# Performance work log

Measured on AMD Instinct MI355X. Metric: run time of the kernel, lower is better.

## Reference

```python
import jax, jax.numpy as jnp
import numpy as np

N_NODES = 100000
N_EDGES = 1600000
D_IN = 128
D_HID = 128
D_OUT = 32


def setup_inputs() -> dict:
    key = jax.random.key(0)
    ks = jax.random.split(key, 10)
    x = jax.random.normal(ks[0], (N_NODES, D_IN), dtype=jnp.float32)
    edge_index = jax.random.randint(ks[1], (2, N_EDGES), 0, N_NODES, dtype=jnp.int64)
    s = 0.05
    return {
        "x": x,
        "edge_index": edge_index,
        "Wl0": jax.random.normal(ks[2], (D_IN, D_HID), jnp.float32) * s,
        "bl0": jnp.zeros((D_HID,), jnp.float32),
        "Wr0": jax.random.normal(ks[3], (D_IN, D_HID), jnp.float32) * s,
        "Wl1": jax.random.normal(ks[4], (D_HID, D_HID), jnp.float32) * s,
        "bl1": jnp.zeros((D_HID,), jnp.float32),
        "Wr1": jax.random.normal(ks[5], (D_HID, D_HID), jnp.float32) * s,
        "Wl2": jax.random.normal(ks[6], (D_HID, D_OUT), jnp.float32) * s,
        "bl2": jnp.zeros((D_OUT,), jnp.float32),
        "Wr2": jax.random.normal(ks[7], (D_HID, D_OUT), jnp.float32) * s,
    }


def _sage_conv(x, src, dst, Wl, bl, Wr):
    # PyG SAGEConv (aggr='mean', root_weight=True):
    # out[i] = lin_l(mean_{j in N(i)} x_j) + lin_r(x_i)
    n = x.shape[0]
    msgs = x[src]                                        # [E, F] gather
    agg = jax.ops.segment_sum(msgs, dst, num_segments=n) # [N, F] scatter-add
    deg = jax.ops.segment_sum(jnp.ones((src.shape[0],), x.dtype), dst, num_segments=n)
    mean = agg / jnp.maximum(deg, 1.0)[:, None]
    return mean @ Wl + bl + x @ Wr


def reference(x, edge_index, Wl0, bl0, Wr0, Wl1, bl1, Wr1, Wl2, bl2, Wr2):
    src, dst = edge_index[0], edge_index[1]
    h = jax.nn.relu(_sage_conv(x, src, dst, Wl0, bl0, Wr0))
    h = jax.nn.relu(_sage_conv(h, src, dst, Wl1, bl1, Wr1))
    h = _sage_conv(h, src, dst, Wl2, bl2, Wr2)
    return jax.nn.log_softmax(h, axis=1)
```

## Files before the change

### kernel.cpp

```cpp
#include <hip/hip_runtime.h>
#include <hip/hip_bf16.h>
#include <math.h>

#define NN 100000
#define NE 1600000

#define NCB 391
#define EB  8192
#define SCT 512

typedef __attribute__((ext_vector_type(8))) short short8;
typedef __attribute__((ext_vector_type(4))) float f32x4;

__device__ __forceinline__ unsigned short f2bf(float f) {
  union { float f; unsigned int i; } v; v.f = f;
  unsigned int i = v.i;
  unsigned int r = (i + 0x7FFFu + ((i >> 16) & 1u)) >> 16;
  return (unsigned short)r;
}
__device__ __forceinline__ float bflo(unsigned int u) {
  union { unsigned int i; float f; } v; v.i = u << 16; return v.f;
}
__device__ __forceinline__ float bfhi(unsigned int u) {
  union { unsigned int i; float f; } v; v.i = u & 0xFFFF0000u; return v.f;
}
__device__ __forceinline__ float bf1(unsigned short u) {
  union { unsigned int i; float f; } v; v.i = ((unsigned int)u) << 16; return v.f;
}

__global__ __launch_bounds__(512) void k_chist(const int* __restrict__ dst,
                                               int* __restrict__ ccnt) {
  __shared__ int h[NCB];
  for (int i = threadIdx.x; i < NCB; i += 512) h[i] = 0;
  __syncthreads();
  int stride = gridDim.x * 512;
  for (int e = blockIdx.x * 512 + threadIdx.x; e < NE; e += stride) {
    int d = dst[e];
    d = d < 0 ? 0 : (d >= NN ? NN - 1 : d);
    atomicAdd(&h[d >> 8], 1);
  }
  __syncthreads();
  for (int i = threadIdx.x; i < NCB; i += 512) {
    int v = h[i];
    if (v) atomicAdd(&ccnt[i], v);
  }
}

__global__ __launch_bounds__(512) void k_cscan(const int* __restrict__ ccnt,
                                               int* __restrict__ cboff,
                                               int* __restrict__ csroff) {
  __shared__ int sd[512];
  int t = threadIdx.x;
  int v = (t < NCB) ? ccnt[t] : 0;
  sd[t] = v;
  __syncthreads();
  for (int st = 1; st < 512; st <<= 1) {
    int x = (t >= st) ? sd[t - st] : 0;
    __syncthreads();
    sd[t] += x;
    __syncthreads();
  }
  if (t < NCB) cboff[t] = sd[t] - v;
  if (t == NCB - 1) { cboff[NCB] = sd[t]; csroff[NN] = sd[t]; }
}

__global__ __launch_bounds__(SCT) void k_cscatter(
    const int* __restrict__ src, const int* __restrict__ dst,
    const int* __restrict__ cboff, int* __restrict__ ccur,
    unsigned int* __restrict__ ebuf) {
  __shared__ int lh[NCB];
  unsigned int cbr[16], pv[16];
  int t = threadIdx.x;
  int base = blockIdx.x * EB;
  for (int i = t; i < NCB; i += SCT) lh[i] = 0;
  __syncthreads();
  #pragma unroll
  for (int i = 0; i < 16; i++) {
    int e = base + i * SCT + t;
    if (e < NE) {
      int d = dst[e];
      d = d < 0 ? 0 : (d >= NN ? NN - 1 : d);
      int s = src[e];
      s = s < 0 ? 0 : (s >= NN ? NN - 1 : s);
      int cb = d >> 8;
      int r = atomicAdd(&lh[cb], 1);
      cbr[i] = (((unsigned int)cb) << 13) | (unsigned int)r;
      pv[i]  = (((unsigned int)(d & 255)) << 17) | (unsigned int)s;
    } else {
      cbr[i] = 0xFFFFFFFFu;
    }
  }
  __syncthreads();
  for (int i = t; i < NCB; i += SCT) {
    int c = lh[i];
    int g = c ? atomicAdd(&ccur[i], c) : 0;
    lh[i] = cboff[i] + g;
  }
  __syncthreads();
  #pragma unroll
  for (int i = 0; i < 16; i++) {
    if (cbr[i] != 0xFFFFFFFFu) {
      int cb = cbr[i] >> 13;
      int r  = cbr[i] & 0x1FFF;
      ebuf[lh[cb] + r] = pv[i];
    }
  }
}

__global__ __launch_bounds__(256) void k_crefine(
    const unsigned int* __restrict__ ebuf, const int* __restrict__ cboff,
    int* __restrict__ csroff, float* __restrict__ invd,
    int* __restrict__ csrsrc) {
  __shared__ int lh[256], pos[256], cur[256];
  int b = blockIdx.x, t = threadIdx.x;
  lh[t] = 0; cur[t] = 0;
  __syncthreads();
  int beg = cboff[b], end = cboff[b + 1];
  for (int i = beg + t; i < end; i += 256) atomicAdd(&lh[ebuf[i] >> 17], 1);
  __syncthreads();
  int v = lh[t];
  pos[t] = v;
  __syncthreads();
  for (int st = 1; st < 256; st <<= 1) {
    int x = (t >= st) ? pos[t - st] : 0;
    __syncthreads();
    pos[t] += x;
    __syncthreads();
  }
  int nid = b * 256 + t;
  int mybase = cboff[b] + pos[t] - v;
  if (nid < NN) {
    csroff[nid] = mybase;
    invd[nid] = 1.0f / (float)(v < 1 ? 1 : v);
  }
  __syncthreads();
  pos[t] = mybase;
  __syncthreads();
  for (int i = beg + t; i < end; i += 256) {
    unsigned int u = ebuf[i];
    int local = u >> 17;
    int r = atomicAdd(&cur[local], 1);
    csrsrc[pos[local] + r] = (int)(u & 0x1FFFFu);
  }
}

__global__ void k_wprep(const float* __restrict__ Wl, const float* __restrict__ Wr,
                        int nch, unsigned short* __restrict__ B) {
  int idx = blockIdx.x * 256 + threadIdx.x;
  int total = 2 * nch * 128;
  if (idx < total) {
    int n = idx >> 7;
    int k = idx & 127;
    float v = (n < nch) ? Wl[k * nch + n] : Wr[k * nch + (n - nch)];
    B[idx] = f2bf(v);
  }
}

template <int NC, int AFP32>
__global__ __launch_bounds__(512) void k_mgemm(
    const void* __restrict__ Ap, const unsigned short* __restrict__ Bp,
    const float* __restrict__ bias,
    unsigned short* __restrict__ yl, unsigned short* __restrict__ yr) {
  __shared__ unsigned short sA[128 * 136];
  __shared__ unsigned short sB[NC * 136];
  int tid = threadIdx.x;
  int nb  = blockIdx.x * 128;

  if (AFP32) {
    const float* A = (const float*)Ap;
    #pragma unroll
    for (int i = 0; i < 8; i++) {
      int j = i * 512 + tid;
      int m = j >> 5;
      int k4 = (j & 31) * 4;
      int gn = nb + m;
      float4 v = make_float4(0.f, 0.f, 0.f, 0.f);
      if (gn < NN) v = *(const float4*)&A[gn * 128 + k4];
      unsigned int p0 = (unsigned int)f2bf(v.x) | ((unsigned int)f2bf(v.y) << 16);
      unsigned int p1 = (unsigned int)f2bf(v.z) | ((unsigned int)f2bf(v.w) << 16);
      *(uint2*)&sA[m * 136 + k4] = make_uint2(p0, p1);
    }
  } else {
    const unsigned short* A = (const unsigned short*)Ap;
    #pragma unroll
    for (int i = 0; i < 4; i++) {
      int j = i * 512 + tid;
      int m = j >> 4;
      int k8 = (j & 15) * 8;
      int gn = nb + m;
      uint4 v = make_uint4(0, 0, 0, 0);
      if (gn < NN) v = *(const uint4*)&A[gn * 128 + k8];
      *(uint4*)&sA[m * 136 + k8] = v;
    }
  }
  {
    int nchunks = NC * 16;
    for (int j = tid; j < nchunks; j += 512) {
      int n = j >> 4;
      int k8 = (j & 15) * 8;
      *(uint4*)&sB[n * 136 + k8] = *(const uint4*)&Bp[n * 128 + k8];
    }
  }
  __syncthreads();

  int wave = tid >> 6, lane = tid & 63;
  int l15 = lane & 15, lq = lane >> 4;
  constexpr int MT = (NC == 256) ? 4 : 2;
  constexpr int NT = (NC == 256) ? 4 : 2;
  int wm, wn;
  if (NC == 256) { wm = wave & 1; wn = wave >> 1; }
  else           { wm = wave >> 1; wn = wave & 1; }
  int mbase = wm * (MT * 16);
  int nbase = wn * (NT * 16);

  f32x4 acc[MT][NT];
  #pragma unroll
  for (int mi = 0; mi < MT; mi++)
    #pragma unroll
    for (int ni = 0; ni < NT; ni++) acc[mi][ni] = (f32x4){0.f, 0.f, 0.f, 0.f};

  #pragma unroll
  for (int kc = 0; kc < 4; kc++) {
    int k0 = kc * 32 + lq * 8;
    short8 af[MT], bfr[NT];
    #pragma unroll
    for (int mi = 0; mi < MT; mi++)
      af[mi] = *(const short8*)&sA[(mbase + mi * 16 + l15) * 136 + k0];
    #pragma unroll
    for (int ni = 0; ni < NT; ni++)
      bfr[ni] = *(const short8*)&sB[(nbase + ni * 16 + l15) * 136 + k0];
    #pragma unroll
    for (int mi = 0; mi < MT; mi++)
      #pragma unroll
      for (int ni = 0; ni < NT; ni++)
        acc[mi][ni] = __builtin_amdgcn_mfma_f32_16x16x32_bf16(
            af[mi], bfr[ni], acc[mi][ni], 0, 0, 0);
  }

  constexpr int HC = NC / 2;
  #pragma unroll
  for (int mi = 0; mi < MT; mi++) {
    #pragma unroll
    for (int ni = 0; ni < NT; ni++) {
      int n = nbase + ni * 16 + l15;
      #pragma unroll
      for (int r = 0; r < 4; r++) {
        int gn = nb + mbase + mi * 16 + lq * 4 + r;
        if (gn < NN) {
          float v = acc[mi][ni][r];
          if (n < HC) {
            yl[(size_t)gn * HC + n] = f2bf(v);
          } else {
            int n2 = n - HC;
            yr[(size_t)gn * HC + n2] = f2bf(v + bias[n2]);
          }
        }
      }
    }
  }
}

__global__ __launch_bounds__(256) void k_agg128(
    const unsigned short* __restrict__ yl, const unsigned short* __restrict__ yr,
    const int* __restrict__ off, const int* __restrict__ csr,
    const float* __restrict__ invd, unsigned short* __restrict__ out, int relu) {
  int wid  = (blockIdx.x * 256 + threadIdx.x) >> 6;
  int lane = threadIdx.x & 63;
  if (wid >= NN) return;
  int beg = off[wid], end = off[wid + 1];
  const unsigned int* ylp = (const unsigned int*)yl;
  float ax0 = 0.f, ay0 = 0.f, ax1 = 0.f, ay1 = 0.f;
  float ax2 = 0.f, ay2 = 0.f, ax3 = 0.f, ay3 = 0.f;
  int e = beg;
  for (; e + 7 < end; e += 8) {
    int s0 = csr[e],     s1 = csr[e + 1], s2 = csr[e + 2], s3 = csr[e + 3];
    int s4 = csr[e + 4], s5 = csr[e + 5], s6 = csr[e + 6], s7 = csr[e + 7];
    unsigned int u0 = ylp[s0 * 64 + lane];
    unsigned int u1 = ylp[s1 * 64 + lane];
    unsigned int u2 = ylp[s2 * 64 + lane];
    unsigned int u3 = ylp[s3 * 64 + lane];
    unsigned int u4 = ylp[s4 * 64 + lane];
    unsigned int u5 = ylp[s5 * 64 + lane];
    unsigned int u6 = ylp[s6 * 64 + lane];
    unsigned int u7 = ylp[s7 * 64 + lane];
    ax0 += bflo(u0); ay0 += bfhi(u0);
    ax1 += bflo(u1); ay1 += bfhi(u1);
    ax2 += bflo(u2); ay2 += bfhi(u2);
    ax3 += bflo(u3); ay3 += bfhi(u3);
    ax0 += bflo(u4); ay0 += bfhi(u4);
    ax1 += bflo(u5); ay1 += bfhi(u5);
    ax2 += bflo(u6); ay2 += bfhi(u6);
    ax3 += bflo(u7); ay3 += bfhi(u7);
  }
  for (; e < end; e++) {
    int s = csr[e];
    unsigned int u = ylp[s * 64 + lane];
    ax0 += bflo(u); ay0 += bfhi(u);
  }
  float sc = invd[wid];
  unsigned int rv = ((const unsigned int*)yr)[wid * 64 + lane];
  float vx = ((ax0 + ax1) + (ax2 + ax3)) * sc + bflo(rv);
  float vy = ((ay0 + ay1) + (ay2 + ay3)) * sc + bfhi(rv);
  if (relu) { vx = fmaxf(vx, 0.f); vy = fmaxf(vy, 0.f); }
  ((unsigned int*)out)[wid * 64 + lane] =
      (unsigned int)f2bf(vx) | ((unsigned int)f2bf(vy) << 16);
}

__global__ __launch_bounds__(256) void k_agg32_lsm(
    const unsigned short* __restrict__ yl, const unsigned short* __restrict__ yr,
    const int* __restrict__ off, const int* __restrict__ csr,
    const float* __restrict__ invd, float* __restrict__ out) {
  int row  = (blockIdx.x * 256 + threadIdx.x) >> 5;
  int lane = threadIdx.x & 31;
  if (row >= NN) return;
  int beg = off[row], end = off[row + 1];
  float a0 = 0.f, a1 = 0.f, a2 = 0.f, a3 = 0.f;
  int e = beg;
  for (; e + 3 < end; e += 4) {
    int s0 = csr[e], s1 = csr[e + 1], s2 = csr[e + 2], s3 = csr[e + 3];
    a0 += bf1(yl[s0 * 32 + lane]);
    a1 += bf1(yl[s1 * 32 + lane]);
    a2 += bf1(yl[s2 * 32 + lane]);
    a3 += bf1(yl[s3 * 32 + lane]);
  }
  for (; e < end; e++) a0 += bf1(yl[csr[e] * 32 + lane]);
  float v = ((a0 + a1) + (a2 + a3)) * invd[row] + bf1(yr[row * 32 + lane]);
  float m = v;
  #pragma unroll
  for (int o = 16; o; o >>= 1) m = fmaxf(m, __shfl_xor(m, o, 32));
  float ex = expf(v - m);
  float s = ex;
  #pragma unroll
  for (int o = 16; o; o >>= 1) s += __shfl_xor(s, o, 32);
  out[row * 32 + lane] = v - m - logf(s);
}


extern "C" void kernel_launch(void* const* d_in, const int* in_sizes, int n_in,
                              void* d_out, int out_size, void* d_ws, size_t ws_size,
                              hipStream_t stream) {
  (void)in_sizes; (void)n_in; (void)out_size; (void)ws_size;
  const float* x   = (const float*)d_in[0];
  const int*   ei  = (const int*)d_in[1];
  const float* Wl0 = (const float*)d_in[2];
  const float* bl0 = (const float*)d_in[3];
  const float* Wr0 = (const float*)d_in[4];
  const float* Wl1 = (const float*)d_in[5];
  const float* bl1 = (const float*)d_in[6];
  const float* Wr1 = (const float*)d_in[7];
  const float* Wl2 = (const float*)d_in[8];
  const float* bl2 = (const float*)d_in[9];
  const float* Wr2 = (const float*)d_in[10];
  const int* srcI = ei;
  const int* dstI = ei + NE;

  char* w = (char*)d_ws;
  int*   ccnt   = (int*)(w + 0);
  int*   ccur   = (int*)(w + (16 << 10));
  int*   cboff  = (int*)(w + (32 << 10));
  unsigned short* B0 = (unsigned short*)(w + (64 << 10));
  unsigned short* B1 = (unsigned short*)(w + (160 << 10));
  unsigned short* B2 = (unsigned short*)(w + (256 << 10));
  int*   csroff = (int*)(w + (512 << 10));
  float* invd   = (float*)(w + (1024 << 10));
  unsigned int* ebuf = (unsigned int*)(w + (size_t)(2) * 1024 * 1024);
  int*   csrsrc = (int*)(w + (size_t)(9) * 1024 * 1024);
  unsigned short* ylb = (unsigned short*)(w + (size_t)(16) * 1024 * 1024);
  unsigned short* yrb = (unsigned short*)(w + (size_t)(48) * 1024 * 1024);
  unsigned short* hb  = (unsigned short*)(w + (size_t)(80) * 1024 * 1024);

  hipMemsetAsync(ccnt, 0, NCB * sizeof(int), stream);
  hipMemsetAsync(ccur, 0, NCB * sizeof(int), stream);

  k_chist<<<128, 512, 0, stream>>>(dstI, ccnt);
  k_cscan<<<1, 512, 0, stream>>>(ccnt, cboff, csroff);
  k_cscatter<<<(NE + EB - 1) / EB, SCT, 0, stream>>>(srcI, dstI, cboff, ccur, ebuf);
  k_crefine<<<NCB, 256, 0, stream>>>(ebuf, cboff, csroff, invd, csrsrc);

  k_wprep<<<(2 * 128 * 128 + 255) / 256, 256, 0, stream>>>(Wl0, Wr0, 128, B0);
  k_wprep<<<(2 * 128 * 128 + 255) / 256, 256, 0, stream>>>(Wl1, Wr1, 128, B1);
  k_wprep<<<(2 * 32 * 128 + 255) / 256, 256, 0, stream>>>(Wl2, Wr2, 32, B2);

  dim3 gg((NN + 127) / 128);
  k_mgemm<256, 1><<<gg, 512, 0, stream>>>(x, B0, bl0, ylb, yrb);
  k_agg128<<<(NN * 64) / 256, 256, 0, stream>>>(ylb, yrb, csroff, csrsrc, invd, hb, 1);
  k_mgemm<256, 0><<<gg, 512, 0, stream>>>(hb, B1, bl1, ylb, yrb);
  k_agg128<<<(NN * 64) / 256, 256, 0, stream>>>(ylb, yrb, csroff, csrsrc, invd, hb, 1);
  k_mgemm<64, 0><<<gg, 512, 0, stream>>>(hb, B2, bl2, ylb, yrb);
  k_agg32_lsm<<<(NN * 32) / 256, 256, 0, stream>>>(ylb, yrb, csroff, csrsrc, invd,
                                                   (float*)d_out);
}
```

Before: 485.4 us.

## Drop memsets via per-block histograms, merge weight prep, deepen gather unroll

Each histogram block now writes its own partial counts, which the scan kernel sums. The scan kernel also zeroes the cursor array, so both memsets and the global atomics go away. The three weight-prep launches become one. The scatter kernel keeps its rank and payload in shared memory instead of registers. The aggregation kernels unroll the neighbour gather to 16 (or 8), use nontemporal loads for CSR indices and nontemporal stores for outputs, trading register/LDS pressure for more loads in flight.

Result: slower. 497.7 us (+2.5%).

```diff
diff --git a/kernel.cpp b/kernel.cpp
--- a/kernel.cpp
+++ b/kernel.cpp
@@ -8,6 +8,7 @@
 #define NCB 391
 #define EB  8192
 #define SCT 512
+#define HBK 128
 
 typedef __attribute__((ext_vector_type(8))) short short8;
 typedef __attribute__((ext_vector_type(4))) float f32x4;
@@ -29,29 +30,39 @@
 }
 
 __global__ __launch_bounds__(512) void k_chist(const int* __restrict__ dst,
-                                               int* __restrict__ ccnt) {
+                                               int* __restrict__ part) {
   __shared__ int h[NCB];
   for (int i = threadIdx.x; i < NCB; i += 512) h[i] = 0;
   __syncthreads();
-  int stride = gridDim.x * 512;
+  int stride = HBK * 512;
   for (int e = blockIdx.x * 512 + threadIdx.x; e < NE; e += stride) {
     int d = dst[e];
     d = d < 0 ? 0 : (d >= NN ? NN - 1 : d);
     atomicAdd(&h[d >> 8], 1);
   }
   __syncthreads();
-  for (int i = threadIdx.x; i < NCB; i += 512) {
-    int v = h[i];
-    if (v) atomicAdd(&ccnt[i], v);
-  }
-}
-
-__global__ __launch_bounds__(512) void k_cscan(const int* __restrict__ ccnt,
+  for (int i = threadIdx.x; i < NCB; i += 512) part[blockIdx.x * NCB + i] = h[i];
+}
+
+__global__ __launch_bounds__(512) void k_cscan(const int* __restrict__ part,
                                                int* __restrict__ cboff,
+                                               int* __restrict__ ccur,
                                                int* __restrict__ csroff) {
   __shared__ int sd[512];
   int t = threadIdx.x;
-  int v = (t < NCB) ? ccnt[t] : 0;
+  int v = 0;
+  if (t < NCB) {
+    int s0 = 0, s1 = 0, s2 = 0, s3 = 0;
+    #pragma unroll 4
+    for (int k = 0; k < HBK; k += 4) {
+      s0 += part[(k + 0) * NCB + t];
+      s1 += part[(k + 1) * NCB + t];
+      s2 += part[(k + 2) * NCB + t];
+      s3 += part[(k + 3) * NCB + t];
+    }
+    v = (s0 + s1) + (s2 + s3);
+    ccur[t] = 0;
+  }
   sd[t] = v;
   __syncthreads();
   for (int st = 1; st < 512; st <<= 1) {
@@ -69,14 +80,17 @@
     const int* __restrict__ cboff, int* __restrict__ ccur,
     unsigned int* __restrict__ ebuf) {
   __shared__ int lh[NCB];
-  unsigned int cbr[16], pv[16];
+  __shared__ unsigned int sRank[EB];
+  __shared__ unsigned int sPay[EB];
   int t = threadIdx.x;
   int base = blockIdx.x * EB;
   for (int i = t; i < NCB; i += SCT) lh[i] = 0;
   __syncthreads();
   #pragma unroll
-  for (int i = 0; i < 16; i++) {
-    int e = base + i * SCT + t;
+  for (int i = 0; i < EB / SCT; i++) {
+    int idx = i * SCT + t;
+    int e = base + idx;
+    unsigned int rk = 0xFFFFFFFFu, pv = 0;
     if (e < NE) {
       int d = dst[e];
       d = d < 0 ? 0 : (d >= NN ? NN - 1 : d);
@@ -84,11 +98,11 @@
       s = s < 0 ? 0 : (s >= NN ? NN - 1 : s);
       int cb = d >> 8;
       int r = atomicAdd(&lh[cb], 1);
-      cbr[i] = (((unsigned int)cb) << 13) | (unsigned int)r;
-      pv[i]  = (((unsigned int)(d & 255)) << 17) | (unsigned int)s;
-    } else {
-      cbr[i] = 0xFFFFFFFFu;
-    }
+      rk = (((unsigned int)cb) << 13) | (unsigned int)r;
+      pv = (((unsigned int)(d & 255)) << 17) | (unsigned int)s;
+    }
+    sRank[idx] = rk;
+    sPay[idx]  = pv;
   }
   __syncthreads();
   for (int i = t; i < NCB; i += SCT) {
@@ -98,11 +112,13 @@
   }
   __syncthreads();
   #pragma unroll
-  for (int i = 0; i < 16; i++) {
-    if (cbr[i] != 0xFFFFFFFFu) {
-      int cb = cbr[i] >> 13;
-      int r  = cbr[i] & 0x1FFF;
-      ebuf[lh[cb] + r] = pv[i];
+  for (int i = 0; i < EB / SCT; i++) {
+    int idx = i * SCT + t;
+    unsigned int rk = sRank[idx];
+    if (rk != 0xFFFFFFFFu) {
+      int cb = rk >> 13;
+      int r  = rk & 0x1FFF;
+      ebuf[lh[cb] + r] = sPay[idx];
     }
   }
 }
@@ -144,15 +160,27 @@
   }
 }
 
-__global__ void k_wprep(const float* __restrict__ Wl, const float* __restrict__ Wr,
-                        int nch, unsigned short* __restrict__ B) {
+__global__ void k_wprep(const float* __restrict__ Wl0, const float* __restrict__ Wr0,
+                        const float* __restrict__ Wl1, const float* __restrict__ Wr1,
+                        const float* __restrict__ Wl2, const float* __restrict__ Wr2,
+                        unsigned short* __restrict__ B0,
+                        unsigned short* __restrict__ B1,
+                        unsigned short* __restrict__ B2) {
   int idx = blockIdx.x * 256 + threadIdx.x;
-  int total = 2 * nch * 128;
-  if (idx < total) {
-    int n = idx >> 7;
-    int k = idx & 127;
-    float v = (n < nch) ? Wl[k * nch + n] : Wr[k * nch + (n - nch)];
-    B[idx] = f2bf(v);
+  if (idx < 32768) {
+    int n = idx >> 7, k = idx & 127;
+    float v = (n < 128) ? Wl0[k * 128 + n] : Wr0[k * 128 + (n - 128)];
+    B0[idx] = f2bf(v);
+  } else if (idx < 65536) {
+    int j = idx - 32768;
+    int n = j >> 7, k = j & 127;
+    float v = (n < 128) ? Wl1[k * 128 + n] : Wr1[k * 128 + (n - 128)];
+    B1[j] = f2bf(v);
+  } else if (idx < 73728) {
+    int j = idx - 65536;
+    int n = j >> 7, k = j & 127;
+    float v = (n < 32) ? Wl2[k * 32 + n] : Wr2[k * 32 + (n - 32)];
+    B2[j] = f2bf(v);
   }
 }
 
@@ -272,25 +300,35 @@
   float ax0 = 0.f, ay0 = 0.f, ax1 = 0.f, ay1 = 0.f;
   float ax2 = 0.f, ay2 = 0.f, ax3 = 0.f, ay3 = 0.f;
   int e = beg;
+  for (; e + 15 < end; e += 16) {
+    int s[16];
+    #pragma unroll
+    for (int i = 0; i < 16; i++) s[i] = __builtin_nontemporal_load(&csr[e + i]);
+    unsigned int u[16];
+    #pragma unroll
+    for (int i = 0; i < 16; i++) u[i] = ylp[s[i] * 64 + lane];
+    #pragma unroll
+    for (int i = 0; i < 16; i += 4) {
+      ax0 += bflo(u[i + 0]); ay0 += bfhi(u[i + 0]);
+      ax1 += bflo(u[i + 1]); ay1 += bfhi(u[i + 1]);
+      ax2 += bflo(u[i + 2]); ay2 += bfhi(u[i + 2]);
+      ax3 += bflo(u[i + 3]); ay3 += bfhi(u[i + 3]);
+    }
+  }
   for (; e + 7 < end; e += 8) {
-    int s0 = csr[e],     s1 = csr[e + 1], s2 = csr[e + 2], s3 = csr[e + 3];
-    int s4 = csr[e + 4], s5 = csr[e + 5], s6 = csr[e + 6], s7 = csr[e + 7];
-    unsigned int u0 = ylp[s0 * 64 + lane];
-    unsigned int u1 = ylp[s1 * 64 + lane];
-    unsigned int u2 = ylp[s2 * 64 + lane];
-    unsigned int u3 = ylp[s3 * 64 + lane];
-    unsigned int u4 = ylp[s4 * 64 + lane];
-    unsigned int u5 = ylp[s5 * 64 + lane];
-    unsigned int u6 = ylp[s6 * 64 + lane];
-    unsigned int u7 = ylp[s7 * 64 + lane];
-    ax0 += bflo(u0); ay0 += bfhi(u0);
-    ax1 += bflo(u1); ay1 += bfhi(u1);
-    ax2 += bflo(u2); ay2 += bfhi(u2);
-    ax3 += bflo(u3); ay3 += bfhi(u3);
-    ax0 += bflo(u4); ay0 += bfhi(u4);
-    ax1 += bflo(u5); ay1 += bfhi(u5);
-    ax2 += bflo(u6); ay2 += bfhi(u6);
-    ax3 += bflo(u7); ay3 += bfhi(u7);
+    int s[8];
+    #pragma unroll
+    for (int i = 0; i < 8; i++) s[i] = __builtin_nontemporal_load(&csr[e + i]);
+    unsigned int u[8];
+    #pragma unroll
+    for (int i = 0; i < 8; i++) u[i] = ylp[s[i] * 64 + lane];
+    #pragma unroll
+    for (int i = 0; i < 8; i += 4) {
+      ax0 += bflo(u[i + 0]); ay0 += bfhi(u[i + 0]);
+      ax1 += bflo(u[i + 1]); ay1 += bfhi(u[i + 1]);
+      ax2 += bflo(u[i + 2]); ay2 += bfhi(u[i + 2]);
+      ax3 += bflo(u[i + 3]); ay3 += bfhi(u[i + 3]);
+    }
   }
   for (; e < end; e++) {
     int s = csr[e];
@@ -302,8 +340,8 @@
   float vx = ((ax0 + ax1) + (ax2 + ax3)) * sc + bflo(rv);
   float vy = ((ay0 + ay1) + (ay2 + ay3)) * sc + bfhi(rv);
   if (relu) { vx = fmaxf(vx, 0.f); vy = fmaxf(vy, 0.f); }
-  ((unsigned int*)out)[wid * 64 + lane] =
-      (unsigned int)f2bf(vx) | ((unsigned int)f2bf(vy) << 16);
+  unsigned int ov = (unsigned int)f2bf(vx) | ((unsigned int)f2bf(vy) << 16);
+  __builtin_nontemporal_store(ov, &((unsigned int*)out)[wid * 64 + lane]);
 }
 
 __global__ __launch_bounds__(256) void k_agg32_lsm(
@@ -316,12 +354,14 @@
   int beg = off[row], end = off[row + 1];
   float a0 = 0.f, a1 = 0.f, a2 = 0.f, a3 = 0.f;
   int e = beg;
-  for (; e + 3 < end; e += 4) {
-    int s0 = csr[e], s1 = csr[e + 1], s2 = csr[e + 2], s3 = csr[e + 3];
-    a0 += bf1(yl[s0 * 32 + lane]);
-    a1 += bf1(yl[s1 * 32 + lane]);
-    a2 += bf1(yl[s2 * 32 + lane]);
-    a3 += bf1(yl[s3 * 32 + lane]);
+  for (; e + 7 < end; e += 8) {
+    int s[8];
+    #pragma unroll
+    for (int i = 0; i < 8; i++) s[i] = __builtin_nontemporal_load(&csr[e + i]);
+    a0 += bf1(yl[s[0] * 32 + lane]) + bf1(yl[s[4] * 32 + lane]);
+    a1 += bf1(yl[s[1] * 32 + lane]) + bf1(yl[s[5] * 32 + lane]);
+    a2 += bf1(yl[s[2] * 32 + lane]) + bf1(yl[s[6] * 32 + lane]);
+    a3 += bf1(yl[s[3] * 32 + lane]) + bf1(yl[s[7] * 32 + lane]);
   }
   for (; e < end; e++) a0 += bf1(yl[csr[e] * 32 + lane]);
   float v = ((a0 + a1) + (a2 + a3)) * invd[row] + bf1(yr[row * 32 + lane]);
@@ -332,7 +372,7 @@
   float s = ex;
   #pragma unroll
   for (int o = 16; o; o >>= 1) s += __shfl_xor(s, o, 32);
-  out[row * 32 + lane] = v - m - logf(s);
+  __builtin_nontemporal_store(v - m - logf(s), &out[row * 32 + lane]);
 }
 
 
@@ -355,12 +395,12 @@
   const int* dstI = ei + NE;
 
   char* w = (char*)d_ws;
-  int*   ccnt   = (int*)(w + 0);
   int*   ccur   = (int*)(w + (16 << 10));
   int*   cboff  = (int*)(w + (32 << 10));
   unsigned short* B0 = (unsigned short*)(w + (64 << 10));
   unsigned short* B1 = (unsigned short*)(w + (160 << 10));
   unsigned short* B2 = (unsigned short*)(w + (256 << 10));
+  int*   part   = (int*)(w + (288 << 10));
   int*   csroff = (int*)(w + (512 << 10));
   float* invd   = (float*)(w + (1024 << 10));
   unsigned int* ebuf = (unsigned int*)(w + (size_t)(2) * 1024 * 1024);
@@ -369,17 +409,13 @@
   unsigned short* yrb = (unsigned short*)(w + (size_t)(48) * 1024 * 1024);
   unsigned short* hb  = (unsigned short*)(w + (size_t)(80) * 1024 * 1024);
 
-  hipMemsetAsync(ccnt, 0, NCB * sizeof(int), stream);
-  hipMemsetAsync(ccur, 0, NCB * sizeof(int), stream);
-
-  k_chist<<<128, 512, 0, stream>>>(dstI, ccnt);
-  k_cscan<<<1, 512, 0, stream>>>(ccnt, cboff, csroff);
+  k_chist<<<HBK, 512, 0, stream>>>(dstI, part);
+  k_cscan<<<1, 512, 0, stream>>>(part, cboff, ccur, csroff);
   k_cscatter<<<(NE + EB - 1) / EB, SCT, 0, stream>>>(srcI, dstI, cboff, ccur, ebuf);
   k_crefine<<<NCB, 256, 0, stream>>>(ebuf, cboff, csroff, invd, csrsrc);
 
-  k_wprep<<<(2 * 128 * 128 + 255) / 256, 256, 0, stream>>>(Wl0, Wr0, 128, B0);
-  k_wprep<<<(2 * 128 * 128 + 255) / 256, 256, 0, stream>>>(Wl1, Wr1, 128, B1);
-  k_wprep<<<(2 * 32 * 128 + 255) / 256, 256, 0, stream>>>(Wl2, Wr2, 32, B2);
+  k_wprep<<<(73728 + 255) / 256, 256, 0, stream>>>(Wl0, Wr0, Wl1, Wr1, Wl2, Wr2,
+                                                   B0, B1, B2);
 
   dim3 gg((NN + 127) / 128);
   k_mgemm<256, 1><<<gg, 512, 0, stream>>>(x, B0, bl0, ylb, yrb);
```
